# Kernel tuning notes

Measured on AMD Instinct MI355X. Metric: run time of the kernel, lower is better.

The kernel has to match this reference:

```python
import jax, jax.numpy as jnp
import numpy as np

FONT_NUM = 190
HID = 256
HEADS = 2
EPS = 1e-5


def _bn(x, g, b, m, v):
    # eval-mode BatchNorm over the last (channel) axis
    return (x - m) * (g * jax.lax.rsqrt(v + EPS)) + b


def _gru(x, Wih, Whh, bih, bhh):
    # x: [B, S, D]; PyTorch gate order r, z, n. Returns all hidden states [B, S, H].
    B, S, _ = x.shape
    H = Whh.shape[1]
    xp = x @ Wih.T + bih  # [B, S, 3H] -- one big GEMM for all timesteps
    def step(h, xt):
        gh = h @ Whh.T + bhh
        xr, xz, xn = jnp.split(xt, 3, axis=-1)
        hr, hz, hn = jnp.split(gh, 3, axis=-1)
        r = jax.nn.sigmoid(xr + hr)
        z = jax.nn.sigmoid(xz + hz)
        n = jnp.tanh(xn + r * hn)
        h_new = (1.0 - z) * n + z * h
        return h_new, h_new
    h0 = jnp.zeros((B, H), x.dtype)
    _, hs = jax.lax.scan(step, h0, jnp.swapaxes(xp, 0, 1))
    return jnp.swapaxes(hs, 0, 1)


def _forward(img_emb, text_embs, len_mask, label_mask, labels,
             img_W, img_b, img_g, img_beta, img_m, img_v,
             g1_Wih, g1_Whh, g1_bih, g1_bhh, tl_W, tl_b,
             t_g, t_beta, t_m, t_v,
             g2_Wih, g2_Whh, g2_bih, g2_bhh, cl_W, cl_b,
             c_g, c_beta, c_m, c_v,
             attn_Win, attn_bin, attn_Wout, attn_bout, pred_W, pred_b):
    # img encoder: Linear -> BN -> (Dropout eval=id) -> ReLU
    img_fea = jax.nn.relu(_bn(img_emb @ img_W.T + img_b, img_g, img_beta, img_m, img_v))  # [B,H]
    # text encoder: GRU -> ReLU -> Linear, then BN+ReLU (torch does this in [B,C,S]; equivalent over channels)
    t = jax.nn.relu(_gru(text_embs, g1_Wih, g1_Whh, g1_bih, g1_bhh))
    t = t @ tl_W.T + tl_b
    text_fea = jax.nn.relu(_bn(t, t_g, t_beta, t_m, t_v))  # [B,S,H]
    len_info = len_mask.sum(axis=1)  # [B]
    # NOTE: sum over ALL timesteps divided by valid length (faithful to source)
    mean = text_fea.sum(axis=1) / len_info[:, None]  # [B,H]
    contrast = text_fea - mean[:, None, :]
    c = jax.nn.relu(_gru(contrast, g2_Wih, g2_Whh, g2_bih, g2_bhh))
    c = c @ cl_W.T + cl_b
    contrast_fea = jax.nn.relu(_bn(c, c_g, c_beta, c_m, c_v))  # [B,S,H]
    B, S, H = text_fea.shape
    hd = H // HEADS
    # batched 3-token self-attention: collapse the per-timestep python loop into one call
    tokens = jnp.stack([
        jnp.broadcast_to(img_fea[:, None, :], (B, S, H)), text_fea, contrast_fea
    ], axis=0).reshape(3, B * S, H)  # [3, N, H]
    Wq, Wk, Wv = jnp.split(attn_Win, 3, axis=0)
    bq, bk, bv = jnp.split(attn_bin, 3, axis=0)
    scale = 1.0 / jnp.sqrt(jnp.asarray(hd, tokens.dtype))
    q = (tokens @ Wq.T + bq).reshape(3, B * S, HEADS, hd) * scale
    k = (tokens @ Wk.T + bk).reshape(3, B * S, HEADS, hd)
    v = (tokens @ Wv.T + bv).reshape(3, B * S, HEADS, hd)
    scores = jnp.einsum('tnhd,snhd->nhts', q, k)  # [N, heads, 3, 3]
    attn = jax.nn.softmax(scores, axis=-1)
    o = jnp.einsum('nhts,snhd->tnhd', attn, v).reshape(3, B * S, H)
    o = o @ attn_Wout.T + attn_bout
    last = o.mean(axis=0).reshape(B, S, H)  # att_fea.mean(0) over the 3 tokens
    logits = last @ pred_W.T + pred_b  # [B,S,FONT_NUM]
    pred = jax.nn.softmax(logits, axis=-1)
    oh = jnp.maximum(label_mask, jax.nn.one_hot(labels, FONT_NUM, dtype=pred.dtype))
    loss = -(oh * jnp.log(pred)).sum(axis=-1)  # [B,S]
    loss = (loss * len_mask).sum(axis=1) / len_info
    return loss.mean()


def setup_inputs() -> dict:
    key = jax.random.key(0)
    ks = jax.random.split(key, 16)
    B, S, D, H = 128, 128, 2048, HID
    img_emb = jax.random.normal(ks[0], (B, D), jnp.float32)
    text_embs = jax.random.normal(ks[1], (B, S, D), jnp.float32)
    lengths = jax.random.randint(ks[2], (B,), S // 2, S + 1)
    len_mask = (jnp.arange(S)[None, :] < lengths[:, None]).astype(jnp.float32)
    labels = jax.random.randint(ks[3], (B, S), 0, FONT_NUM)
    label_mask = jnp.zeros((B, S, FONT_NUM), jnp.float32)
    w = lambda k, sh: jax.random.normal(k, sh, jnp.float32) * 0.02
    params = dict(
        img_W=w(ks[4], (H, D)), img_b=jnp.zeros((H,)),
        img_g=jnp.ones((H,)), img_beta=jnp.zeros((H,)), img_m=jnp.zeros((H,)), img_v=jnp.ones((H,)),
        g1_Wih=w(ks[5], (3 * (H // 2), D)), g1_Whh=w(ks[6], (3 * (H // 2), H // 2)),
        g1_bih=jnp.zeros((3 * (H // 2),)), g1_bhh=jnp.zeros((3 * (H // 2),)),
        tl_W=w(ks[7], (H, H // 2)), tl_b=jnp.zeros((H,)),
        t_g=jnp.ones((H,)), t_beta=jnp.zeros((H,)), t_m=jnp.zeros((H,)), t_v=jnp.ones((H,)),
        g2_Wih=w(ks[8], (3 * H, H)), g2_Whh=w(ks[9], (3 * H, H)),
        g2_bih=jnp.zeros((3 * H,)), g2_bhh=jnp.zeros((3 * H,)),
        cl_W=w(ks[10], (H, H)), cl_b=jnp.zeros((H,)),
        c_g=jnp.ones((H,)), c_beta=jnp.zeros((H,)), c_m=jnp.zeros((H,)), c_v=jnp.ones((H,)),
        attn_Win=w(ks[11], (3 * H, H)), attn_bin=jnp.zeros((3 * H,)),
        attn_Wout=w(ks[12], (H, H)), attn_bout=jnp.zeros((H,)),
        pred_W=w(ks[13], (FONT_NUM, H)), pred_b=jnp.zeros((FONT_NUM,)),
    )
    return dict(img_emb=img_emb, text_embs=text_embs, len_mask=len_mask,
                label_mask=label_mask, labels=labels, **params)


def reference(img_emb, text_embs, len_mask, label_mask, labels,
              img_W, img_b, img_g, img_beta, img_m, img_v,
              g1_Wih, g1_Whh, g1_bih, g1_bhh, tl_W, tl_b,
              t_g, t_beta, t_m, t_v,
              g2_Wih, g2_Whh, g2_bih, g2_bhh, cl_W, cl_b,
              c_g, c_beta, c_m, c_v,
              attn_Win, attn_bin, attn_Wout, attn_bout, pred_W, pred_b):
    return _forward(img_emb, text_embs, len_mask, label_mask, labels,
                    img_W, img_b, img_g, img_beta, img_m, img_v,
                    g1_Wih, g1_Whh, g1_bih, g1_bhh, tl_W, tl_b,
                    t_g, t_beta, t_m, t_v,
                    g2_Wih, g2_Whh, g2_bih, g2_bhh, cl_W, cl_b,
                    c_g, c_beta, c_m, c_v,
                    attn_Win, attn_bin, attn_Wout, attn_bout, pred_W, pred_b)
```

## Files before the change

kernel.cpp:

```cpp
#include <hip/hip_runtime.h>

typedef __attribute__((ext_vector_type(8))) short short8;
typedef __attribute__((ext_vector_type(4))) float f32x4;
typedef _Float16 f16;
typedef __attribute__((ext_vector_type(2))) _Float16 f16x2;
typedef __attribute__((ext_vector_type(8))) _Float16 f16x8;

__device__ inline float bf2f(unsigned short u){
  union{float f; unsigned u32;} x; x.u32 = ((unsigned)u) << 16; return x.f;
}
__device__ inline unsigned short f2bf(float f){
  union{float f; unsigned u;} x; x.f = f;
  unsigned r = (x.u + 0x7FFFu + ((x.u >> 16) & 1u)) >> 16;
  return (unsigned short)r;
}

#if defined(__has_builtin)
#  if __has_builtin(__builtin_amdgcn_fdot2)
#    define HAS_FDOT2 1
#  endif
#endif
__device__ inline float dot2f(f16x2 a, f16x2 b, float c){
#ifdef HAS_FDOT2
  return __builtin_amdgcn_fdot2(a, b, c, false);
#else
  return c + (float)a.x * (float)b.x + (float)a.y * (float)b.y;
#endif
}
__device__ inline f16x2 asf16x2(int v){ return __builtin_bit_cast(f16x2, v); }
__device__ inline int pack2(float lo, float hi){
  f16x2 p = f16x2{(f16)lo, (f16)hi};
  return __builtin_bit_cast(int, p);
}

__device__ inline float sigmoidf_(float x){ return 1.f / (1.f + __expf(-x)); }
__device__ inline float tanh_fast(float x){ float e = __expf(2.f * x); return 1.f - 2.f / (e + 1.f); }

__device__ inline float dpp_xor1(float x){
  return __int_as_float(__builtin_amdgcn_update_dpp(0, __float_as_int(x), 0xB1, 0xF, 0xF, true));
}
__device__ inline float dpp_xor2(float x){
  return __int_as_float(__builtin_amdgcn_update_dpp(0, __float_as_int(x), 0x4E, 0xF, 0xF, true));
}

__device__ inline void load8bf(const unsigned short* p, float* o){
  uint4 q = *(const uint4*)p;
  o[0]=bf2f((unsigned short)(q.x & 0xffffu)); o[1]=bf2f((unsigned short)(q.x >> 16));
  o[2]=bf2f((unsigned short)(q.y & 0xffffu)); o[3]=bf2f((unsigned short)(q.y >> 16));
  o[4]=bf2f((unsigned short)(q.z & 0xffffu)); o[5]=bf2f((unsigned short)(q.z >> 16));
  o[6]=bf2f((unsigned short)(q.w & 0xffffu)); o[7]=bf2f((unsigned short)(q.w >> 16));
}

#define GLL16(g, l) __builtin_amdgcn_global_load_lds(                      \
    (const __attribute__((address_space(1))) void*)(g),                    \
    (__attribute__((address_space(3))) void*)(l), 16, 0, 0)

__global__ __launch_bounds__(256) void conv_bf16_k(const float* __restrict__ src,
                                                   unsigned short* __restrict__ dst, int n4){
  int i = blockIdx.x * 256 + threadIdx.x;
  if (i >= n4) return;
  float4 v = ((const float4*)src)[i];
  union { unsigned short s[4]; uint2 q; } u;
  u.s[0]=f2bf(v.x); u.s[1]=f2bf(v.y); u.s[2]=f2bf(v.z); u.s[3]=f2bf(v.w);
  ((uint2*)dst)[i] = u.q;
}

__global__ __launch_bounds__(256) void conv_f16_k(const float* __restrict__ src,
                                                  f16* __restrict__ dst, int n4){
  int i = blockIdx.x * 256 + threadIdx.x;
  if (i >= n4) return;
  float4 v = ((const float4*)src)[i];
  union { f16 s[4]; uint2 q; } u;
  u.s[0]=(f16)v.x; u.s[1]=(f16)v.y; u.s[2]=(f16)v.z; u.s[3]=(f16)v.w;
  ((uint2*)dst)[i] = u.q;
}

__global__ __launch_bounds__(256) void pred_pad_k(const float* __restrict__ W,
                                                  const float* __restrict__ b,
                                                  unsigned short* __restrict__ Wd,
                                                  float* __restrict__ bd){
  int i = blockIdx.x * 256 + threadIdx.x;
  int j = i >> 8;
  Wd[i] = (j < 190) ? f2bf(W[i]) : (unsigned short)0;
  if (i < 192) bd[i] = (i < 190) ? b[i] : 0.f;
}

template<int OUT_T, bool BN, bool AF32>
__global__ __launch_bounds__(256) void gemm128_k(
    const void* __restrict__ Ap, const unsigned short* __restrict__ Bw,
    const float* __restrict__ bias,
    const float* __restrict__ gam, const float* __restrict__ bet,
    const float* __restrict__ mu,  const float* __restrict__ var,
    void* __restrict__ Cp, int M, int N, int K)
{
  __shared__ __align__(16) unsigned short As[4096];
  __shared__ __align__(16) unsigned short Bs[4096];
  const int tid  = threadIdx.x;
  const int lane = tid & 63, wid = tid >> 6;
  const int wm = wid & 1, wn = wid >> 1;
  const int bm = blockIdx.y << 7, bn = blockIdx.x << 7;
  const int rA = tid >> 2, seg = tid & 3;

  f32x4 acc[4][4];
  #pragma unroll
  for (int i = 0; i < 4; i++)
    #pragma unroll
    for (int j = 0; j < 4; j++)
      acc[i][j] = f32x4{0.f, 0.f, 0.f, 0.f};

  const unsigned short* Abf = (const unsigned short*)Ap;
  const float* Af = (const float*)Ap;
  char* asb = (char*)As;
  char* bsb = (char*)Bs;
  char* asw = asb + wid * 1024;
  char* bsw = bsb + wid * 1024;

  for (int k0 = 0; k0 < K; k0 += 32) {
    if (AF32) {
      #pragma unroll
      for (int beta = 0; beta < 2; beta++) {
        const float* src = Af + (size_t)(bm + rA + beta * 64) * K + k0 + seg * 8;
        float4 v0 = *(const float4*)src;
        float4 v1 = *(const float4*)(src + 4);
        union { unsigned short s[8]; uint4 q; } u;
        u.s[0]=f2bf(v0.x); u.s[1]=f2bf(v0.y); u.s[2]=f2bf(v0.z); u.s[3]=f2bf(v0.w);
        u.s[4]=f2bf(v1.x); u.s[5]=f2bf(v1.y); u.s[6]=f2bf(v1.z); u.s[7]=f2bf(v1.w);
        *(uint4*)(asb + beta * 4096 + tid * 16) = u.q;
      }
    } else {
      GLL16(Abf + (size_t)(bm + rA)      * K + k0 + seg * 8, asw);
      GLL16(Abf + (size_t)(bm + rA + 64) * K + k0 + seg * 8, asw + 4096);
    }
    GLL16(Bw + (size_t)(bn + rA)      * K + k0 + seg * 8, bsw);
    GLL16(Bw + (size_t)(bn + rA + 64) * K + k0 + seg * 8, bsw + 4096);
    __syncthreads();

    short8 a[4], b[4];
    #pragma unroll
    for (int f = 0; f < 4; f++) {
      int ra = wm * 64 + f * 16 + (lane & 15);
      a[f] = *(const short8*)(asb + ra * 64 + (lane >> 4) * 16);
      int rb = wn * 64 + f * 16 + (lane & 15);
      b[f] = *(const short8*)(bsb + rb * 64 + (lane >> 4) * 16);
    }
    #pragma unroll
    for (int fm = 0; fm < 4; fm++)
      #pragma unroll
      for (int fn = 0; fn < 4; fn++)
        acc[fm][fn] = __builtin_amdgcn_mfma_f32_16x16x32_bf16(a[fm], b[fn], acc[fm][fn], 0, 0, 0);
    __syncthreads();
  }

  #pragma unroll
  for (int fn = 0; fn < 4; fn++) {
    int col = bn + wn * 64 + fn * 16 + (lane & 15);
    float bs = bias[col];
    float sc = 1.f, sh = 0.f;
    if (BN) { float s = gam[col] * rsqrtf(var[col] + 1e-5f); sc = s; sh = bet[col] - mu[col] * s; }
    #pragma unroll
    for (int fm = 0; fm < 4; fm++) {
      int row = bm + wm * 64 + fm * 16 + ((lane >> 4) << 2);
      #pragma unroll
      for (int j = 0; j < 4; j++) {
        float v = acc[fm][fn][j] + bs;
        if (BN) { v = v * sc + sh; v = fmaxf(v, 0.f); }
        size_t idx = (size_t)(row + j) * N + col;
        if (OUT_T == 1) ((f16*)Cp)[idx] = (f16)v;
        else            ((unsigned short*)Cp)[idx] = f2bf(v);
      }
    }
  }
}

template<int OUT_T, bool BN, bool AF32>
__global__ __launch_bounds__(256) void gemm_k(
    const void* __restrict__ Ap, const unsigned short* __restrict__ Bw,
    const float* __restrict__ bias,
    const float* __restrict__ gam, const float* __restrict__ bet,
    const float* __restrict__ mu,  const float* __restrict__ var,
    void* __restrict__ Cp, int M, int N, int K)
{
  __shared__ unsigned short As[64][40];
  __shared__ unsigned short Bs[64][40];
  const int tid  = threadIdx.x;
  const int lane = tid & 63, wid = tid >> 6;
  const int wm = wid & 1, wn = wid >> 1;
  const int bm = blockIdx.y << 6, bn = blockIdx.x << 6;
  const int srow = tid >> 2, sseg = tid & 3;

  f32x4 acc[2][2];
  #pragma unroll
  for (int i = 0; i < 2; i++)
    #pragma unroll
    for (int j = 0; j < 2; j++)
      acc[i][j] = f32x4{0.f, 0.f, 0.f, 0.f};

  const unsigned short* Abf = (const unsigned short*)Ap;
  const float* Af = (const float*)Ap;

  for (int k0 = 0; k0 < K; k0 += 32) {
    if (AF32) {
      const float* src = Af + (size_t)(bm + srow) * K + k0 + sseg * 8;
      float4 v0 = *(const float4*)(src);
      float4 v1 = *(const float4*)(src + 4);
      union { unsigned short s[8]; uint4 q; } u;
      u.s[0]=f2bf(v0.x); u.s[1]=f2bf(v0.y); u.s[2]=f2bf(v0.z); u.s[3]=f2bf(v0.w);
      u.s[4]=f2bf(v1.x); u.s[5]=f2bf(v1.y); u.s[6]=f2bf(v1.z); u.s[7]=f2bf(v1.w);
      *(uint4*)&As[srow][sseg * 8] = u.q;
    } else {
      *(uint4*)&As[srow][sseg * 8] =
          *(const uint4*)(Abf + (size_t)(bm + srow) * K + k0 + sseg * 8);
    }
    *(uint4*)&Bs[srow][sseg * 8] =
        *(const uint4*)(Bw + (size_t)(bn + srow) * K + k0 + sseg * 8);
    __syncthreads();

    short8 a0 = *(const short8*)&As[wm * 32 +      (lane & 15)][(lane >> 4) * 8];
    short8 a1 = *(const short8*)&As[wm * 32 + 16 + (lane & 15)][(lane >> 4) * 8];
    short8 b0 = *(const short8*)&Bs[wn * 32 +      (lane & 15)][(lane >> 4) * 8];
    short8 b1 = *(const short8*)&Bs[wn * 32 + 16 + (lane & 15)][(lane >> 4) * 8];
    acc[0][0] = __builtin_amdgcn_mfma_f32_16x16x32_bf16(a0, b0, acc[0][0], 0, 0, 0);
    acc[0][1] = __builtin_amdgcn_mfma_f32_16x16x32_bf16(a0, b1, acc[0][1], 0, 0, 0);
    acc[1][0] = __builtin_amdgcn_mfma_f32_16x16x32_bf16(a1, b0, acc[1][0], 0, 0, 0);
    acc[1][1] = __builtin_amdgcn_mfma_f32_16x16x32_bf16(a1, b1, acc[1][1], 0, 0, 0);
    __syncthreads();
  }

  #pragma unroll
  for (int fn = 0; fn < 2; fn++) {
    int col = bn + wn * 32 + fn * 16 + (lane & 15);
    float bs = bias[col];
    float sc = 1.f, sh = 0.f;
    if (BN) { float s = gam[col] * rsqrtf(var[col] + 1e-5f); sc = s; sh = bet[col] - mu[col] * s; }
    #pragma unroll
    for (int fm = 0; fm < 2; fm++) {
      int row = bm + wm * 32 + fm * 16 + ((lane >> 4) << 2);
      #pragma unroll
      for (int j = 0; j < 4; j++) {
        float v = acc[fm][fn][j] + bs;
        if (BN) { v = v * sc + sh; v = fmaxf(v, 0.f); }
        size_t idx = (size_t)(row + j) * N + col;
        if (OUT_T == 0)      ((float*)Cp)[idx] = v;
        else if (OUT_T == 1) ((f16*)Cp)[idx]   = (f16)v;
        else                 ((unsigned short*)Cp)[idx] = f2bf(v);
      }
    }
  }
}

__global__ __launch_bounds__(512, 2) void gru2_scan_k(
    const f16* __restrict__ Wf,
    const float* __restrict__ bhh,
    const f16* __restrict__ xp, unsigned short* __restrict__ hs_relu)
{
  const int b = blockIdx.x;
  const int tid = threadIdx.x;
  const int jj = tid >> 1, kh = tid & 1;
  __shared__ __align__(16) f16 hbuf[2][272];
  __shared__ __align__(16) char wnl[16 * 512 * 16];

  {
    const f16* src = Wf + (size_t)(512 + jj) * 256 + kh * 128;
    #pragma unroll
    for (int c = 0; c < 16; c++)
      *(uint4*)(wnl + c * 8192 + tid * 16) = *(const uint4*)(src + c * 8);
  }

  int wri[64];
  #pragma unroll
  for (int i = 0; i < 16; i++) {
    uint4 q = *(const uint4*)&Wf[(size_t)jj * 256 + kh * 128 + i * 8];
    wri[4*i+0] = (int)q.x; wri[4*i+1] = (int)q.y; wri[4*i+2] = (int)q.z; wri[4*i+3] = (int)q.w;
  }
  #pragma unroll
  for (int i = 0; i < 64; i++)
    asm volatile("" : "+v"(wri[i]));

  const f16* zsrc = Wf + (size_t)(256 + jj) * 256 + kh * 128;

  const float br = bhh[jj], bz = bhh[jj + 256], bn2 = bhh[jj + 512];
  if (tid < 256) hbuf[0][(tid & 127) + (tid >> 7) * 136] = (f16)0.f;
  float hprev = 0.f;
  f16 pxr = (f16)0.f, pxz = (f16)0.f, pxn = (f16)0.f;
  if (kh == 0) {
    const f16* x0 = xp + (size_t)(b * 128) * 768;
    pxr = x0[jj]; pxz = x0[256 + jj]; pxn = x0[512 + jj];
  }
  __syncthreads();
  int cur = 0;
  const char* mynb = wnl + tid * 16;
  for (int t = 0; t < 128; t++) {
    float xr = (float)pxr, xz = (float)pxz, xn = (float)pxn;
    if (kh == 0) {
      const int tn = (t < 127) ? (t + 1) : 127;
      const f16* xnr = xp + (size_t)(b * 128 + tn) * 768;
      pxr = xnr[jj]; pxz = xnr[256 + jj]; pxn = xnr[512 + jj];
    }
    uint4 zb[8];
    #pragma unroll
    for (int c = 0; c < 8; c++) zb[c] = *(const uint4*)(zsrc + c * 8);

    const char* hb = (const char*)hbuf[cur] + kh * 272;
    float ar = 0.f, az = 0.f, an = 0.f;
    #pragma unroll
    for (int i = 0; i < 16; i++) {
      f16x8 hv = *(const f16x8*)(hb + i * 16);
      f16x8 wv = *(const f16x8*)(mynb + i * 8192);
      f16x8 zv = __builtin_bit_cast(f16x8, zb[i & 7]);
      if (i < 8) zb[i] = *(const uint4*)(zsrc + (i + 8) * 8);
      #pragma unroll
      for (int u = 0; u < 4; u++) {
        f16x2 hp = f16x2{hv[2*u], hv[2*u+1]};
        ar = dot2f(asf16x2(wri[4*i+u]), hp, ar);
        az = dot2f(f16x2{zv[2*u], zv[2*u+1]}, hp, az);
        an = dot2f(f16x2{wv[2*u], wv[2*u+1]}, hp, an);
      }
    }
    ar += dpp_xor1(ar);
    az += dpp_xor1(az);
    an += dpp_xor1(an);
    if (kh == 0) {
      float r = sigmoidf_(xr + ar + br);
      float z = sigmoidf_(xz + az + bz);
      float n = tanh_fast(xn + r * (an + bn2));
      float hnew = (1.f - z) * n + z * hprev;
      hprev = hnew;
      hbuf[cur ^ 1][(jj & 127) + (jj >> 7) * 136] = (f16)hnew;
      hs_relu[(size_t)(b * 128 + t) * 256 + jj] = f2bf(fmaxf(hnew, 0.f));
    }
    __syncthreads();
    cur ^= 1;
  }
}

__global__ __launch_bounds__(512, 4) void gru1_scan_k(
    const float* __restrict__ Whh, const float* __restrict__ bhh,
    const f16* __restrict__ xp, unsigned short* __restrict__ hs_relu)
{
  const int b = blockIdx.x;
  const int tid = threadIdx.x;
  const int jj = tid >> 2, kh = tid & 3;
  __shared__ __align__(16) f16 hbuf[2][128];

  int wri[16], wzi[16], wni[16];
  #pragma unroll
  for (int i = 0; i < 4; i++) {
    const int kb = kh * 32 + i * 8;
    float4 f0, f1;
    f0 = *(const float4*)&Whh[(size_t)(jj      ) * 128 + kb];
    f1 = *(const float4*)&Whh[(size_t)(jj      ) * 128 + kb + 4];
    wri[4*i+0] = pack2(f0.x, f0.y); wri[4*i+1] = pack2(f0.z, f0.w);
    wri[4*i+2] = pack2(f1.x, f1.y); wri[4*i+3] = pack2(f1.z, f1.w);
    f0 = *(const float4*)&Whh[(size_t)(jj + 128) * 128 + kb];
    f1 = *(const float4*)&Whh[(size_t)(jj + 128) * 128 + kb + 4];
    wzi[4*i+0] = pack2(f0.x, f0.y); wzi[4*i+1] = pack2(f0.z, f0.w);
    wzi[4*i+2] = pack2(f1.x, f1.y); wzi[4*i+3] = pack2(f1.z, f1.w);
    f0 = *(const float4*)&Whh[(size_t)(jj + 256) * 128 + kb];
    f1 = *(const float4*)&Whh[(size_t)(jj + 256) * 128 + kb + 4];
    wni[4*i+0] = pack2(f0.x, f0.y); wni[4*i+1] = pack2(f0.z, f0.w);
    wni[4*i+2] = pack2(f1.x, f1.y); wni[4*i+3] = pack2(f1.z, f1.w);
  }
  #pragma unroll
  for (int i = 0; i < 16; i++)
    asm volatile("" : "+v"(wri[i]), "+v"(wzi[i]), "+v"(wni[i]));

  const float br = bhh[jj], bz = bhh[jj + 128], bn2 = bhh[jj + 256];
  if (tid < 128) hbuf[0][tid] = (f16)0.f;
  float hprev = 0.f;
  f16 pxr = (f16)0.f, pxz = (f16)0.f, pxn = (f16)0.f;
  if (kh == 0) {
    const f16* x0 = xp + (size_t)(b * 128) * 384;
    pxr = x0[jj]; pxz = x0[128 + jj]; pxn = x0[256 + jj];
  }
  __syncthreads();
  int cur = 0;
  for (int t = 0; t < 128; t++) {
    float xr = (float)pxr, xz = (float)pxz, xn = (float)pxn;
    if (kh == 0) {
      const int tn = (t < 127) ? (t + 1) : 127;
      const f16* xnr = xp + (size_t)(b * 128 + tn) * 384;
      pxr = xnr[jj]; pxz = xnr[128 + jj]; pxn = xnr[256 + jj];
    }
    const char* hb = (const char*)hbuf[cur] + kh * 64;
    float ar = 0.f, az = 0.f, an = 0.f;
    #pragma unroll
    for (int c = 0; c < 4; c++) {
      f16x8 hv = *(const f16x8*)(hb + c * 16);
      #pragma unroll
      for (int u = 0; u < 4; u++) {
        f16x2 hp = f16x2{hv[2*u], hv[2*u+1]};
        ar = dot2f(asf16x2(wri[4*c+u]), hp, ar);
        az = dot2f(asf16x2(wzi[4*c+u]), hp, az);
        an = dot2f(asf16x2(wni[4*c+u]), hp, an);
      }
    }
    ar += dpp_xor1(ar); ar += dpp_xor2(ar);
    az += dpp_xor1(az); az += dpp_xor2(az);
    an += dpp_xor1(an); an += dpp_xor2(an);
    if (kh == 0) {
      float r = sigmoidf_(xr + ar + br);
      float z = sigmoidf_(xz + az + bz);
      float n = tanh_fast(xn + r * (an + bn2));
      float hnew = (1.f - z) * n + z * hprev;
      hprev = hnew;
      hbuf[cur ^ 1][jj] = (f16)hnew;
      hs_relu[(size_t)(b * 128 + t) * 128 + jj] = f2bf(fmaxf(hnew, 0.f));
    }
    __syncthreads();
    cur ^= 1;
  }
}

__global__ __launch_bounds__(256) void mean_k(const unsigned short* __restrict__ tf,
                                              const float* __restrict__ len_mask,
                                              float* __restrict__ mean,
                                              float* __restrict__ len_info){
  int b = blockIdx.x, c = threadIdx.x;
  float acc = 0.f;
  for (int s = 0; s < 128; s++) acc += bf2f(tf[(size_t)(b * 128 + s) * 256 + c]);
  float len = 0.f;
  for (int s = 0; s < 128; s++) len += len_mask[b * 128 + s];
  mean[b * 256 + c] = acc / len;
  if (c == 0) len_info[b] = len;
}

__global__ __launch_bounds__(256) void contrast_k(const unsigned short* __restrict__ tf,
                                                  const float* __restrict__ mean,
                                                  unsigned short* __restrict__ out){
  size_t i = (size_t)blockIdx.x * 256 + threadIdx.x;
  int c = (int)(i & 255);
  int b = (int)(i >> 15);
  out[i] = f2bf(bf2f(tf[i]) - mean[b * 256 + c]);
}

__global__ __launch_bounds__(256) void attn_k(const unsigned short* __restrict__ qkv0,
                                              const unsigned short* __restrict__ qkv1,
                                              const unsigned short* __restrict__ qkv2,
                                              unsigned short* __restrict__ osum){
  int i = blockIdx.x * 256 + threadIdx.x;
  int h = i & 1; int n = i >> 1; int b = n >> 7;
  const unsigned short* t0 = qkv0 + (size_t)b * 768 + h * 128;
  const unsigned short* t1 = qkv1 + (size_t)n * 768 + h * 128;
  const unsigned short* t2 = qkv2 + (size_t)n * 768 + h * 128;
  float sc[3][3];
  #pragma unroll
  for (int a = 0; a < 3; a++)
    #pragma unroll
    for (int s = 0; s < 3; s++) sc[a][s] = 0.f;
  #pragma unroll 1
  for (int dc = 0; dc < 16; dc++) {
    float q[3][8], k[3][8];
    load8bf(t0 + dc * 8, q[0]); load8bf(t1 + dc * 8, q[1]); load8bf(t2 + dc * 8, q[2]);
    load8bf(t0 + 256 + dc * 8, k[0]); load8bf(t1 + 256 + dc * 8, k[1]); load8bf(t2 + 256 + dc * 8, k[2]);
    #pragma unroll
    for (int a = 0; a < 3; a++)
      #pragma unroll
      for (int s = 0; s < 3; s++) {
        float d = 0.f;
        #pragma unroll
        for (int e = 0; e < 8; e++) d += q[a][e] * k[s][e];
        sc[a][s] += d;
      }
  }
  const float scale = 0.08838834764831845f;
  float w[3] = {0.f, 0.f, 0.f};
  #pragma unroll
  for (int a = 0; a < 3; a++) {
    float s0 = sc[a][0] * scale, s1 = sc[a][1] * scale, s2 = sc[a][2] * scale;
    float m = fmaxf(s0, fmaxf(s1, s2));
    float e0 = __expf(s0 - m), e1 = __expf(s1 - m), e2 = __expf(s2 - m);
    float inv = 1.f / (e0 + e1 + e2);
    w[0] += e0 * inv; w[1] += e1 * inv; w[2] += e2 * inv;
  }
  w[0] *= (1.f / 3.f); w[1] *= (1.f / 3.f); w[2] *= (1.f / 3.f);
  unsigned short* op = osum + (size_t)n * 256 + h * 128;
  #pragma unroll 1
  for (int dc = 0; dc < 16; dc++) {
    float v0[8], v1[8], v2[8];
    load8bf(t0 + 512 + dc * 8, v0); load8bf(t1 + 512 + dc * 8, v1); load8bf(t2 + 512 + dc * 8, v2);
    union { unsigned short s[8]; uint4 q; } u;
    #pragma unroll
    for (int e = 0; e < 8; e++) u.s[e] = f2bf(w[0] * v0[e] + w[1] * v1[e] + w[2] * v2[e]);
    *(uint4*)(op + dc * 8) = u.q;
  }
}

__global__ __launch_bounds__(64) void loss_k(const float* __restrict__ logits,
                                             const float* __restrict__ label_mask,
                                             const int* __restrict__ labels,
                                             float* __restrict__ loss_raw){
  int r = blockIdx.x; int j = threadIdx.x;
  int lab = labels[r];
  float l[3]; float m = -1e30f;
  #pragma unroll
  for (int q = 0; q < 3; q++) {
    int c = j + q * 64;
    float lv = (c < 190) ? logits[(size_t)r * 192 + c] : -1e30f;
    l[q] = lv; m = fmaxf(m, lv);
  }
  #pragma unroll
  for (int off = 32; off; off >>= 1) m = fmaxf(m, __shfl_xor(m, off));
  float se = 0.f, soh = 0.f, dot = 0.f;
  #pragma unroll
  for (int q = 0; q < 3; q++) {
    int c = j + q * 64;
    if (c < 190) {
      se += expf(l[q] - m);
      float oh = fmaxf(label_mask[(size_t)r * 190 + c], (c == lab) ? 1.f : 0.f);
      soh += oh; dot += oh * l[q];
    }
  }
  #pragma unroll
  for (int off = 32; off; off >>= 1) {
    se += __shfl_xor(se, off); soh += __shfl_xor(soh, off); dot += __shfl_xor(dot, off);
  }
  if (j == 0) loss_raw[r] = (m + logf(se)) * soh - dot;
}

__global__ __launch_bounds__(256) void final_k(const float* __restrict__ loss_raw,
                                               const float* __restrict__ len_mask,
                                               const float* __restrict__ len_info,
                                               float* __restrict__ out){
  __shared__ float sh[256];
  int t = threadIdx.x;
  float acc = 0.f;
  for (int i = t; i < 16384; i += 256) acc += loss_raw[i] * len_mask[i] / len_info[i >> 7];
  sh[t] = acc; __syncthreads();
  for (int s = 128; s; s >>= 1) { if (t < s) sh[t] += sh[t + s]; __syncthreads(); }
  if (t == 0) out[0] = sh[0] / 128.f;
}

extern "C" void kernel_launch(void* const* d_in, const int* in_sizes, int n_in,
                              void* d_out, int out_size, void* d_ws, size_t ws_size,
                              hipStream_t stream)
{
  const float* img_emb    = (const float*)d_in[0];
  const float* text_embs  = (const float*)d_in[1];
  const float* len_mask   = (const float*)d_in[2];
  const float* label_mask = (const float*)d_in[3];
  const int*   labels     = (const int*)  d_in[4];
  const float* img_W   = (const float*)d_in[5];
  const float* img_b   = (const float*)d_in[6];
  const float* img_g   = (const float*)d_in[7];
  const float* img_be  = (const float*)d_in[8];
  const float* img_m   = (const float*)d_in[9];
  const float* img_v   = (const float*)d_in[10];
  const float* g1_Wih  = (const float*)d_in[11];
  const float* g1_Whh  = (const float*)d_in[12];
  const float* g1_bih  = (const float*)d_in[13];
  const float* g1_bhh  = (const float*)d_in[14];
  const float* tl_W    = (const float*)d_in[15];
  const float* tl_b    = (const float*)d_in[16];
  const float* t_g     = (const float*)d_in[17];
  const float* t_be    = (const float*)d_in[18];
  const float* t_m     = (const float*)d_in[19];
  const float* t_v     = (const float*)d_in[20];
  const float* g2_Wih  = (const float*)d_in[21];
  const float* g2_Whh  = (const float*)d_in[22];
  const float* g2_bih  = (const float*)d_in[23];
  const float* g2_bhh  = (const float*)d_in[24];
  const float* cl_W    = (const float*)d_in[25];
  const float* cl_b    = (const float*)d_in[26];
  const float* c_g     = (const float*)d_in[27];
  const float* c_be    = (const float*)d_in[28];
  const float* c_m     = (const float*)d_in[29];
  const float* c_v     = (const float*)d_in[30];
  const float* a_Win   = (const float*)d_in[31];
  const float* a_bin   = (const float*)d_in[32];
  const float* a_Wout  = (const float*)d_in[33];
  const float* a_bout  = (const float*)d_in[34];
  const float* pred_W  = (const float*)d_in[35];
  const float* pred_b  = (const float*)d_in[36];

  char* ws = (char*)d_ws;
  size_t o = 0;
  auto alloc = [&](size_t sz){ size_t r = o; o += (sz + 255) & ~(size_t)255; return r; };

  size_t o_g1Wih = alloc(384ull*2048*2);
  size_t o_tlW   = alloc(256ull*128*2);
  size_t o_g2Wih = alloc(768ull*256*2);
  size_t o_g2Whh = alloc(768ull*256*2);
  size_t o_clW   = alloc(256ull*256*2);
  size_t o_aWin  = alloc(768ull*256*2);
  size_t o_aWout = alloc(256ull*256*2);
  size_t o_imgW  = alloc(256ull*2048*2);
  size_t o_predW = alloc(192ull*256*2);
  size_t o_predb = alloc(192ull*4);
  size_t o_imgfea= alloc(128ull*256*2);
  size_t o_mean  = alloc(128ull*256*4);
  size_t o_len   = alloc(128ull*4);
  size_t o_R0    = alloc(33554432ull);
  size_t o_RB    = alloc(25165824ull);
  size_t o_tfea  = alloc(16384ull*256*2);
  size_t o_qkv1  = alloc(16384ull*768*2);
  size_t o_cfea  = alloc(16384ull*256*2);
  size_t o_qkv0  = alloc(128ull*768*2);
  size_t o_loss  = alloc(16384ull*4);
  (void)ws_size; (void)in_sizes; (void)n_in; (void)out_size;

  unsigned short* g1Wih_bf = (unsigned short*)(ws + o_g1Wih);
  unsigned short* tlW_bf   = (unsigned short*)(ws + o_tlW);
  unsigned short* g2Wih_bf = (unsigned short*)(ws + o_g2Wih);
  f16*            g2Whh_f  = (f16*)(ws + o_g2Whh);
  unsigned short* clW_bf   = (unsigned short*)(ws + o_clW);
  unsigned short* aWin_bf  = (unsigned short*)(ws + o_aWin);
  unsigned short* aWout_bf = (unsigned short*)(ws + o_aWout);
  unsigned short* imgW_bf  = (unsigned short*)(ws + o_imgW);
  unsigned short* predW_bf = (unsigned short*)(ws + o_predW);
  float*          predb_p  = (float*)(ws + o_predb);
  unsigned short* img_fea  = (unsigned short*)(ws + o_imgfea);
  float*          meanb    = (float*)(ws + o_mean);
  float*          len_info = (float*)(ws + o_len);
  f16*            xp2      = (f16*)(ws + o_R0);
  unsigned short* hs2      = (unsigned short*)(ws + o_R0 + 25165824ull);
  unsigned short* osum     = (unsigned short*)(ws + o_R0);
  unsigned short* lastb    = (unsigned short*)(ws + o_R0 + 8388608ull);
  f16*            xp1      = (f16*)(ws + o_RB);
  unsigned short* hs1      = (unsigned short*)(ws + o_RB + 12582912ull);
  unsigned short* contr    = (unsigned short*)(ws + o_RB + 16777216ull);
  unsigned short* qkv2     = (unsigned short*)(ws + o_RB);
  unsigned short* tfea     = (unsigned short*)(ws + o_tfea);
  unsigned short* qkv1     = (unsigned short*)(ws + o_qkv1);
  float*          logits   = (float*)(ws + o_qkv1);
  unsigned short* cfea     = (unsigned short*)(ws + o_cfea);
  unsigned short* qkv0     = (unsigned short*)(ws + o_qkv0);
  float*          loss_raw = (float*)(ws + o_loss);
  float*          outp     = (float*)d_out;

  conv_bf16_k<<<768, 256, 0, stream>>>(g1_Wih, g1Wih_bf, 196608);
  conv_bf16_k<<<32,  256, 0, stream>>>(tl_W,   tlW_bf,   8192);
  conv_bf16_k<<<192, 256, 0, stream>>>(g2_Wih, g2Wih_bf, 49152);
  conv_f16_k <<<192, 256, 0, stream>>>(g2_Whh, g2Whh_f,  49152);
  conv_bf16_k<<<64,  256, 0, stream>>>(cl_W,   clW_bf,   16384);
  conv_bf16_k<<<192, 256, 0, stream>>>(a_Win,  aWin_bf,  49152);
  conv_bf16_k<<<64,  256, 0, stream>>>(a_Wout, aWout_bf, 16384);
  conv_bf16_k<<<512, 256, 0, stream>>>(img_W,  imgW_bf,  131072);
  pred_pad_k<<<192, 256, 0, stream>>>(pred_W, pred_b, predW_bf, predb_p);

  gemm128_k<2, true, true><<<dim3(2, 1), 256, 0, stream>>>(
      img_emb, imgW_bf, img_b, img_g, img_be, img_m, img_v, img_fea, 128, 256, 2048);

  gemm128_k<1, false, true><<<dim3(3, 128), 256, 0, stream>>>(
      text_embs, g1Wih_bf, g1_bih, nullptr, nullptr, nullptr, nullptr, xp1, 16384, 384, 2048);

  gru1_scan_k<<<128, 512, 0, stream>>>(g1_Whh, g1_bhh, xp1, hs1);

  gemm128_k<2, true, false><<<dim3(2, 128), 256, 0, stream>>>(
      hs1, tlW_bf, tl_b, t_g, t_be, t_m, t_v, tfea, 16384, 256, 128);

  mean_k<<<128, 256, 0, stream>>>(tfea, len_mask, meanb, len_info);
  contrast_k<<<16384, 256, 0, stream>>>(tfea, meanb, contr);

  gemm128_k<1, false, false><<<dim3(6, 128), 256, 0, stream>>>(
      contr, g2Wih_bf, g2_bih, nullptr, nullptr, nullptr, nullptr, xp2, 16384, 768, 256);

  gru2_scan_k<<<128, 512, 0, stream>>>(g2Whh_f, g2_bhh, xp2, hs2);

  gemm128_k<2, true, false><<<dim3(2, 128), 256, 0, stream>>>(
      hs2, clW_bf, cl_b, c_g, c_be, c_m, c_v, cfea, 16384, 256, 256);

  gemm128_k<2, false, false><<<dim3(6, 1), 256, 0, stream>>>(
      img_fea, aWin_bf, a_bin, nullptr, nullptr, nullptr, nullptr, qkv0, 128, 768, 256);
  gemm128_k<2, false, false><<<dim3(6, 128), 256, 0, stream>>>(
      tfea, aWin_bf, a_bin, nullptr, nullptr, nullptr, nullptr, qkv1, 16384, 768, 256);
  gemm128_k<2, false, false><<<dim3(6, 128), 256, 0, stream>>>(
      cfea, aWin_bf, a_bin, nullptr, nullptr, nullptr, nullptr, qkv2, 16384, 768, 256);

  attn_k<<<128, 256, 0, stream>>>(qkv0, qkv1, qkv2, osum);

  gemm128_k<2, false, false><<<dim3(2, 128), 256, 0, stream>>>(
      osum, aWout_bf, a_bout, nullptr, nullptr, nullptr, nullptr, lastb, 16384, 256, 256);

  gemm_k<0, false, false><<<dim3(3, 256), 256, 0, stream>>>(
      lastb, predW_bf, predb_p, nullptr, nullptr, nullptr, nullptr, logits, 16384, 192, 256);

  loss_k<<<16384, 64, 0, stream>>>(logits, label_mask, labels, loss_raw);
  final_k<<<1, 256, 0, stream>>>(loss_raw, len_mask, len_info, outp);
}
```

Baseline: 622.7 us.

## Remap GRU2 scan threads per wave and broadcast hidden state via readlane

Threads in the GRU2 recurrent scan are remapped so that every wave handles a single K-half (kh). Each lane now loads one 16-byte chunk of the hidden state, and `__builtin_amdgcn_readlane` broadcasts it as a scalar operand to the dot2 products. This replaces the per-iteration LDS vector loads of h. Because the two K-halves now sit in different waves, the cross-lane DPP reduction becomes an LDS partial-sum buffer plus an extra `__syncthreads` per timestep. Half the waves also sit idle during the gate activation.

```diff
diff --git a/kernel.cpp b/kernel.cpp
--- a/kernel.cpp
+++ b/kernel.cpp
@@ -255,15 +255,18 @@
 {
   const int b = blockIdx.x;
   const int tid = threadIdx.x;
-  const int jj = tid >> 1, kh = tid & 1;
+  const int w = tid >> 6, lane = tid & 63;
+  const int kh = w & 1;
+  const int jj = (w >> 1) * 64 + lane;
   __shared__ __align__(16) f16 hbuf[2][272];
+  __shared__ __align__(16) float pbuf[256][4];
   __shared__ __align__(16) char wnl[16 * 512 * 16];
 
   {
     const f16* src = Wf + (size_t)(512 + jj) * 256 + kh * 128;
     #pragma unroll
     for (int c = 0; c < 16; c++)
-      *(uint4*)(wnl + c * 8192 + tid * 16) = *(const uint4*)(src + c * 8);
+      *(uint4*)(wnl + c * 8192 + (jj * 2 + kh) * 16) = *(const uint4*)(src + c * 8);
   }
 
   int wri[64];
@@ -288,7 +291,7 @@
   }
   __syncthreads();
   int cur = 0;
-  const char* mynb = wnl + tid * 16;
+  const char* mynb = wnl + (jj * 2 + kh) * 16;
   for (int t = 0; t < 128; t++) {
     float xr = (float)pxr, xz = (float)pxz, xn = (float)pxn;
     if (kh == 0) {
@@ -296,33 +299,44 @@
       const f16* xnr = xp + (size_t)(b * 128 + tn) * 768;
       pxr = xnr[jj]; pxz = xnr[256 + jj]; pxn = xnr[512 + jj];
     }
+    uint4 hreg = *(const uint4*)((const char*)hbuf[cur] + kh * 272 + (lane & 15) * 16);
     uint4 zb[8];
     #pragma unroll
     for (int c = 0; c < 8; c++) zb[c] = *(const uint4*)(zsrc + c * 8);
 
-    const char* hb = (const char*)hbuf[cur] + kh * 272;
     float ar = 0.f, az = 0.f, an = 0.f;
     #pragma unroll
     for (int i = 0; i < 16; i++) {
-      f16x8 hv = *(const f16x8*)(hb + i * 16);
+      int u0 = __builtin_amdgcn_readlane((int)hreg.x, i);
+      int u1 = __builtin_amdgcn_readlane((int)hreg.y, i);
+      int u2 = __builtin_amdgcn_readlane((int)hreg.z, i);
+      int u3 = __builtin_amdgcn_readlane((int)hreg.w, i);
       f16x8 wv = *(const f16x8*)(mynb + i * 8192);
       f16x8 zv = __builtin_bit_cast(f16x8, zb[i & 7]);
       if (i < 8) zb[i] = *(const uint4*)(zsrc + (i + 8) * 8);
-      #pragma unroll
-      for (int u = 0; u < 4; u++) {
-        f16x2 hp = f16x2{hv[2*u], hv[2*u+1]};
-        ar = dot2f(asf16x2(wri[4*i+u]), hp, ar);
-        az = dot2f(f16x2{zv[2*u], zv[2*u+1]}, hp, az);
-        an = dot2f(f16x2{wv[2*u], wv[2*u+1]}, hp, an);
-      }
-    }
-    ar += dpp_xor1(ar);
-    az += dpp_xor1(az);
-    an += dpp_xor1(an);
+      ar = dot2f(asf16x2(wri[4*i+0]), asf16x2(u0), ar);
+      ar = dot2f(asf16x2(wri[4*i+1]), asf16x2(u1), ar);
+      ar = dot2f(asf16x2(wri[4*i+2]), asf16x2(u2), ar);
+      ar = dot2f(asf16x2(wri[4*i+3]), asf16x2(u3), ar);
+      az = dot2f(f16x2{zv[0], zv[1]}, asf16x2(u0), az);
+      az = dot2f(f16x2{zv[2], zv[3]}, asf16x2(u1), az);
+      az = dot2f(f16x2{zv[4], zv[5]}, asf16x2(u2), az);
+      az = dot2f(f16x2{zv[6], zv[7]}, asf16x2(u3), az);
+      an = dot2f(f16x2{wv[0], wv[1]}, asf16x2(u0), an);
+      an = dot2f(f16x2{wv[2], wv[3]}, asf16x2(u1), an);
+      an = dot2f(f16x2{wv[4], wv[5]}, asf16x2(u2), an);
+      an = dot2f(f16x2{wv[6], wv[7]}, asf16x2(u3), an);
+    }
+    if (kh == 1) {
+      f32x4 p = f32x4{ar, az, an, 0.f};
+      *(f32x4*)&pbuf[jj][0] = p;
+    }
+    __syncthreads();
     if (kh == 0) {
-      float r = sigmoidf_(xr + ar + br);
-      float z = sigmoidf_(xz + az + bz);
-      float n = tanh_fast(xn + r * (an + bn2));
+      f32x4 p = *(const f32x4*)&pbuf[jj][0];
+      float r = sigmoidf_(xr + ar + p[0] + br);
+      float z = sigmoidf_(xz + az + p[1] + bz);
+      float n = tanh_fast(xn + r * (an + p[2] + bn2));
       float hnew = (1.f - z) * n + z * hprev;
       hprev = hnew;
       hbuf[cur ^ 1][(jj & 127) + (jj >> 7) * 136] = (f16)hnew;
```

New measurement: 674.6 us. 8.3% more time.
